# Optimization experiments

Hardware: AMD Instinct MI355X
Metric: run time of the kernel (lower is better)

The kernel has to match this reference:

```python
import jax, jax.numpy as jnp
import numpy as np

B, L, D, H, Dh = 4, 2048, 1024, 16, 64
DECAY_LR, A_LR, V_LR, G_LR = 64, 64, 32, 128
EPS_GN = 0.00064


def _lora(x, A, Bm, b, act):
    h = x @ A.T
    if act is not None:
        h = act(h)
    y = h @ Bm.T
    return y if b is None else y + b


def setup_inputs() -> dict:
    key = jax.random.key(0)
    ks = jax.random.split(key, 32)
    n = lambda k, shape, s=0.02: (jax.random.normal(k, shape, jnp.float32) * s)
    return {
        "x": n(ks[0], (B, L, D), 1.0),
        "v_first": n(ks[1], (B, L, H, Dh), 1.0),
        "x_r": n(ks[2], (1, 1, D)), "x_w": n(ks[3], (1, 1, D)),
        "x_k": n(ks[4], (1, 1, D)), "x_v": n(ks[5], (1, 1, D)),
        "x_a": n(ks[6], (1, 1, D)), "x_g": n(ks[7], (1, 1, D)),
        "k_k": n(ks[8], (H, Dh), 0.5), "k_a": n(ks[9], (H, Dh), 0.5),
        "r_k": n(ks[10], (H, Dh), 0.5),
        "Wr": n(ks[11], (D, D)), "Wk": n(ks[12], (D, D)),
        "Wv": n(ks[13], (D, D)), "Wo": n(ks[14], (D, D)),
        "gn_w": 1.0 + n(ks[15], (H, Dh)), "gn_b": n(ks[16], (H, Dh)),
        "w_A": n(ks[17], (DECAY_LR, D)), "w_B": n(ks[18], (D, DECAY_LR)), "w_b": n(ks[19], (D,)),
        "v_A": n(ks[20], (V_LR, D)), "v_B": n(ks[21], (D, V_LR)), "v_b": n(ks[22], (D,)),
        "a_A": n(ks[23], (A_LR, D)), "a_B": n(ks[24], (D, A_LR)), "a_b": n(ks[25], (D,)),
        "g_A": n(ks[26], (G_LR, D)), "g_B": n(ks[27], (D, G_LR)),
    }


def reference(x, v_first, x_r, x_w, x_k, x_v, x_a, x_g, k_k, k_a, r_k,
              Wr, Wk, Wv, Wo, gn_w, gn_b,
              w_A, w_B, w_b, v_A, v_B, v_b, a_A, a_B, a_b, g_A, g_B):
    Bx, Lx, Dx = x.shape
    # token shift (no cache -> zero-padded shift)
    x_prev = jnp.concatenate([jnp.zeros_like(x[:, :1]), x[:, :-1]], axis=1)
    xx = x_prev - x
    xr = x + xx * x_r
    xw = x + xx * x_w
    xk = x + xx * x_k
    xv = x + xx * x_v
    xa = x + xx * x_a
    xg = x + xx * x_g

    r = (xr @ Wr.T).reshape(Bx, Lx, H, Dh)
    k = (xk @ Wk.T).reshape(Bx, Lx, H, Dh)
    v = (xv @ Wv.T).reshape(Bx, Lx, H, Dh)
    iclr = jax.nn.sigmoid(_lora(xa, a_A, a_B, a_b, None)).reshape(Bx, Lx, H, Dh)
    gate = _lora(xg, g_A, g_B, None, jax.nn.sigmoid)  # (B,L,D)

    # layer_idx > 0: residual value mixing with v_first
    vv = jax.nn.sigmoid(_lora(xv, v_A, v_B, v_b, None)).reshape(Bx, Lx, H, Dh)
    v = v + (v_first - v) * vv

    w = jnp.exp(-0.606531 * jax.nn.sigmoid(
        _lora(xw, w_A, w_B, w_b, jnp.tanh)).reshape(Bx, Lx, H, Dh))

    kkn = k * k_k
    kk = kkn / jnp.maximum(jnp.linalg.norm(kkn, axis=-1, keepdims=True), 1e-7)
    k = k * (1.0 + (iclr - 1.0) * k_a)
    a = -kk
    b = kk * iclr

    # WKV7 generalized delta-rule scan over time
    def step(state, inp):
        rt, wt, kt, vt, at, bt = inp  # each (B,H,Dh)
        sa = jnp.einsum('bhij,bhj->bhi', state, at)
        state = (state * wt[:, :, None, :]
                 + vt[..., :, None] * kt[..., None, :]
                 + sa[..., :, None] * bt[..., None, :])
        y = jnp.einsum('bhij,bhj->bhi', state, rt)
        return state, y

    tr = lambda z: jnp.swapaxes(z, 0, 1)  # (B,L,H,Dh) -> (L,B,H,Dh)
    state0 = jnp.zeros((Bx, H, Dh, Dh), x.dtype)
    _, ys = jax.lax.scan(step, state0, (tr(r), tr(w), tr(k), tr(v), tr(a), tr(b)))
    out = jnp.swapaxes(ys, 0, 1)  # (B,L,H,Dh)

    # per-head layernorm (group norm), eps = 0.00064
    mean = out.mean(axis=-1, keepdims=True)
    var = out.var(axis=-1, keepdims=True)
    out = gn_w * (out - mean) / jnp.sqrt(var + EPS_GN) + gn_b

    out = out + jnp.sum(r * k * r_k, axis=-1, keepdims=True) * v
    out = out.reshape(Bx, Lx, Dx)
    return (out * gate) @ Wo.T
```

## Files before the change

### kernel.cpp

```cpp
#include <hip/hip_runtime.h>
#include <cmath>


#define DEV __device__ __forceinline__

typedef unsigned short u16;
typedef unsigned int u32;
typedef __bf16 bf16x8 __attribute__((ext_vector_type(8)));
typedef float f32x4 __attribute__((ext_vector_type(4)));

constexpr int Bx = 4, Lx = 2048, Dx = 1024, Hx = 16, Dh = 64;
constexpr int NTOK = Bx * Lx;
constexpr float EPS_GN = 0.00064f;
constexpr int STEP_U16 = 384;
constexpr int TB = 16;
constexpr int NB = Lx / TB;
constexpr int BATCH_U16 = TB * STEP_U16;

DEV float bf2f(u16 u) { union { u32 i; float f; } c; c.i = ((u32)u) << 16; return c.f; }
DEV u16 f2bf(float f) {
    union { float f; u32 i; } c; c.f = f;
    u32 r = c.i + 0x7FFFu + ((c.i >> 16) & 1u);
    return (u16)(r >> 16);
}
DEV void unpack2(u32 u, float& a, float& b) {
    union { u32 i; float f; } c0, c1;
    c0.i = u << 16; c1.i = u & 0xFFFF0000u;
    a = c0.f; b = c1.f;
}

template <int CTRL>
DEV float dpp_add(float v) {
    int p = __builtin_amdgcn_update_dpp(0, __float_as_int(v), CTRL, 0xF, 0xF, true);
    return v + __int_as_float(p);
}

DEV float xor32_add(float x) {
    float a = x, b = x;
    asm volatile("s_nop 1\n\tv_permlane32_swap_b32 %0, %1" : "+v"(a), "+v"(b));
    return a + b;
}

DEV float red32(float x) {
    x = dpp_add<0xB1>(x);
    x = dpp_add<0x4E>(x);
    x = dpp_add<0x141>(x);
    x = dpp_add<0x140>(x);
    return xor32_add(x);
}

__global__ __launch_bounds__(256) void conv_kernel(
    const float* s0, const float* s1, const float* s2, const float* s3,
    const float* s4, const float* s5, const float* s6, const float* s7,
    const float* s8, const float* s9, const float* s10, const float* s11,
    u16* d0, u16* d1, u16* d2, u16* d3, u16* d4, u16* d5, u16* d6, u16* d7,
    u16* d8, u16* d9, u16* d10, u16* d11)
{
    const float* srcs[12] = {s0,s1,s2,s3,s4,s5,s6,s7,s8,s9,s10,s11};
    u16* dsts[12] = {d0,d1,d2,d3,d4,d5,d6,d7,d8,d9,d10,d11};
    const int ns[12] = {65536,65536,32768,32768,65536,65536,131072,131072,
                        1048576,1048576,1048576,1048576};
    int t = blockIdx.y;
    int i = (blockIdx.x * 256 + threadIdx.x) * 4;
    if (i >= ns[t]) return;
    float4 v = *(const float4*)(srcs[t] + i);
    ushort4 o;
    o.x = f2bf(v.x); o.y = f2bf(v.y); o.z = f2bf(v.z); o.w = f2bf(v.w);
    *(ushort4*)(dsts[t] + i) = o;
}

__global__ __launch_bounds__(256) void mix_kernel(
    const float* __restrict__ x,
    const float* __restrict__ mr, const float* __restrict__ mw, const float* __restrict__ mk,
    const float* __restrict__ mv, const float* __restrict__ ma, const float* __restrict__ mg,
    u16* __restrict__ XR, u16* __restrict__ XW, u16* __restrict__ XK,
    u16* __restrict__ XV, u16* __restrict__ XA, u16* __restrict__ XG)
{
    int gi = blockIdx.x * 256 + threadIdx.x;
    int n  = gi >> 8;
    int d4 = (gi & 255) << 2;
    int l  = n & (Lx - 1);
    size_t o = (size_t)n * Dx + d4;
    float4 xc = *(const float4*)(x + o);
    float4 xp = make_float4(0.f, 0.f, 0.f, 0.f);
    if (l != 0) xp = *(const float4*)(x + o - Dx);
    float dx0 = xp.x - xc.x, dx1 = xp.y - xc.y, dx2 = xp.z - xc.z, dx3 = xp.w - xc.w;
    const float* mvs[6] = {mr, mw, mk, mv, ma, mg};
    u16* dsts[6] = {XR, XW, XK, XV, XA, XG};
#pragma unroll
    for (int j = 0; j < 6; ++j) {
        float4 m = *(const float4*)(mvs[j] + d4);
        ushort4 r;
        r.x = f2bf(fmaf(dx0, m.x, xc.x));
        r.y = f2bf(fmaf(dx1, m.y, xc.y));
        r.z = f2bf(fmaf(dx2, m.z, xc.z));
        r.w = f2bf(fmaf(dx3, m.w, xc.w));
        *(ushort4*)(dsts[j] + o) = r;
    }
}

template <int BN, int ACT, bool BIAS, bool F32OUT>
__global__ __launch_bounds__(256) void gemm_nt(
    const u16* __restrict__ A, const u16* __restrict__ B16,
    const float* __restrict__ bias, void* __restrict__ Cv,
    int M, int N, int K)
{
    constexpr int BM = 128, BK = 32;
    constexpr int LDT = BK + 8;
    constexpr int WGM = (BN == 128) ? 2 : 4;
    constexpr int WGN = (BN == 128) ? 2 : 1;
    constexpr int WTM = BM / WGM, WTN = BN / WGN;
    constexpr int ITM = WTM / 16, ITN = WTN / 16;
    __shared__ __align__(16) u16 Asm[BM * LDT];
    __shared__ __align__(16) u16 Bsm[BN * LDT];
    const int tid = threadIdx.x;
    const int wid = tid >> 6, lane = tid & 63;
    const int q = lane >> 4, r16 = lane & 15;
    const size_t m0 = (size_t)blockIdx.x * BM;
    const size_t n0 = (size_t)blockIdx.y * BN;
    const int wm = (wid % WGM) * WTM;
    const int wn = (wid / WGM) * WTN;
    f32x4 acc[ITM][ITN];
    const f32x4 zf = {0.f, 0.f, 0.f, 0.f};
#pragma unroll
    for (int i = 0; i < ITM; ++i)
#pragma unroll
        for (int j = 0; j < ITN; ++j) acc[i][j] = zf;

    for (int k0 = 0; k0 < K; k0 += BK) {
#pragma unroll
        for (int it = 0; it < (BM * BK) / 2048; ++it) {
            int pp = tid * 8 + it * 2048;
            int row = pp >> 5, col = pp & 31;
            *(uint4*)&Asm[row * LDT + col] = *(const uint4*)(A + (m0 + row) * K + k0 + col);
        }
#pragma unroll
        for (int it = 0; it < (BN * BK + 2047) / 2048; ++it) {
            int pp = tid * 8 + it * 2048;
            if (BN * BK >= 2048 || pp < BN * BK) {
                int row = pp >> 5, col = pp & 31;
                *(uint4*)&Bsm[row * LDT + col] = *(const uint4*)(B16 + (n0 + row) * K + k0 + col);
            }
        }
        __syncthreads();
        bf16x8 af[ITM], bfr[ITN];
#pragma unroll
        for (int im = 0; im < ITM; ++im)
            af[im] = *(const bf16x8*)&Asm[(wm + im * 16 + r16) * LDT + q * 8];
#pragma unroll
        for (int in = 0; in < ITN; ++in)
            bfr[in] = *(const bf16x8*)&Bsm[(wn + in * 16 + r16) * LDT + q * 8];
#pragma unroll
        for (int im = 0; im < ITM; ++im)
#pragma unroll
            for (int in = 0; in < ITN; ++in)
                acc[im][in] = __builtin_amdgcn_mfma_f32_16x16x32_bf16(af[im], bfr[in], acc[im][in], 0, 0, 0);
        __syncthreads();
    }
#pragma unroll
    for (int im = 0; im < ITM; ++im) {
#pragma unroll
        for (int in = 0; in < ITN; ++in) {
#pragma unroll
            for (int e = 0; e < 4; ++e) {
                size_t row = m0 + wm + im * 16 + q * 4 + e;
                size_t col = n0 + wn + in * 16 + r16;
                float val = acc[im][in][e];
                if constexpr (BIAS) val += bias[col];
                if constexpr (ACT == 1) val = 1.f / (1.f + __expf(-val));
                else if constexpr (ACT == 2) val = tanhf(val);
                else if constexpr (ACT == 3) val = __expf(-0.606531f / (1.f + __expf(-val)));
                if constexpr (F32OUT) ((float*)Cv)[row * (size_t)N + col] = val;
                else ((u16*)Cv)[row * (size_t)N + col] = f2bf(val);
            }
        }
    }
}

__global__ __launch_bounds__(256) void lora1_kernel(
    const u16* __restrict__ XW, const u16* __restrict__ XA,
    const u16* __restrict__ XV, const u16* __restrict__ XG,
    const u16* __restrict__ wAB, const u16* __restrict__ aAB,
    const u16* __restrict__ vAB, const u16* __restrict__ gAB,
    u16* __restrict__ HW, u16* __restrict__ HA,
    u16* __restrict__ HV, u16* __restrict__ HG)
{
    constexpr int BM = 128, BN = 64, BK = 32, K = 1024;
    constexpr int LDT = BK + 8;
    constexpr int ITM = 2, ITN = 4;
    const int cfg = blockIdx.y;
    const u16* A; const u16* Bm; u16* C; int ldC, Nv, act;
    if (cfg == 0)      { A = XW; Bm = wAB;            C = HW;      ldC = 64;  Nv = 64; act = 2; }
    else if (cfg == 1) { A = XA; Bm = aAB;            C = HA;      ldC = 64;  Nv = 64; act = 0; }
    else if (cfg == 2) { A = XV; Bm = vAB;            C = HV;      ldC = 32;  Nv = 32; act = 0; }
    else if (cfg == 3) { A = XG; Bm = gAB;            C = HG;      ldC = 128; Nv = 64; act = 1; }
    else               { A = XG; Bm = gAB + 64 * K;   C = HG + 64; ldC = 128; Nv = 64; act = 1; }

    __shared__ __align__(16) u16 Asm[BM * LDT];
    __shared__ __align__(16) u16 Bsm[BN * LDT];
    const int tid = threadIdx.x;
    const int wid = tid >> 6, lane = tid & 63;
    const int q = lane >> 4, r16 = lane & 15;
    const size_t m0 = (size_t)blockIdx.x * BM;
    const int wm = wid * 32;
    f32x4 acc[ITM][ITN];
    const f32x4 zf = {0.f, 0.f, 0.f, 0.f};
#pragma unroll
    for (int i = 0; i < ITM; ++i)
#pragma unroll
        for (int j = 0; j < ITN; ++j) acc[i][j] = zf;

    for (int k0 = 0; k0 < K; k0 += BK) {
#pragma unroll
        for (int it = 0; it < 2; ++it) {
            int pp = tid * 8 + it * 2048;
            int row = pp >> 5, col = pp & 31;
            *(uint4*)&Asm[row * LDT + col] = *(const uint4*)(A + (m0 + row) * K + k0 + col);
        }
        {
            int pp = tid * 8;
            int row = pp >> 5, col = pp & 31;
            *(uint4*)&Bsm[row * LDT + col] = *(const uint4*)(Bm + row * K + k0 + col);
        }
        __syncthreads();
        bf16x8 af[ITM], bfr[ITN];
#pragma unroll
        for (int im = 0; im < ITM; ++im)
            af[im] = *(const bf16x8*)&Asm[(wm + im * 16 + r16) * LDT + q * 8];
#pragma unroll
        for (int in = 0; in < ITN; ++in)
            bfr[in] = *(const bf16x8*)&Bsm[(in * 16 + r16) * LDT + q * 8];
#pragma unroll
        for (int im = 0; im < ITM; ++im)
#pragma unroll
            for (int in = 0; in < ITN; ++in)
                acc[im][in] = __builtin_amdgcn_mfma_f32_16x16x32_bf16(af[im], bfr[in], acc[im][in], 0, 0, 0);
        __syncthreads();
    }
#pragma unroll
    for (int im = 0; im < ITM; ++im) {
#pragma unroll
        for (int in = 0; in < ITN; ++in) {
#pragma unroll
            for (int e = 0; e < 4; ++e) {
                size_t row = m0 + wm + im * 16 + q * 4 + e;
                int col = in * 16 + r16;
                if (col < Nv) {
                    float val = acc[im][in][e];
                    if (act == 1) val = 1.f / (1.f + __expf(-val));
                    else if (act == 2) val = tanhf(val);
                    C[row * (size_t)ldC + col] = f2bf(val);
                }
            }
        }
    }
}

__global__ __launch_bounds__(256) void prep_pack_kernel(
    u16* __restrict__ Kb, u16* __restrict__ Vb,
    const u16* __restrict__ Rb, const u16* __restrict__ Wd16,
    const u16* __restrict__ ICLR, const u16* __restrict__ VVb, const float* __restrict__ vfirst,
    const float* __restrict__ k_k, const float* __restrict__ k_a,
    u16* __restrict__ stream)
{
    int g = blockIdx.x * 4 + (threadIdx.x >> 6);
    int lane = threadIdx.x & 63;
    int h = g & (Hx - 1);
    int n = g >> 4;
    size_t idx = (size_t)g * 64 + lane;
    int hd = h * 64 + lane;
    int l = n & (Lx - 1), b = n >> 11;
    size_t so = ((size_t)((b * 16 + h) * Lx + l)) * STEP_U16;

    float k = bf2f(Kb[idx]);
    float iclr = bf2f(ICLR[idx]);
    float kkn = k * k_k[hd];
    float s = kkn * kkn;
#pragma unroll
    for (int off = 32; off > 0; off >>= 1) s += __shfl_xor(s, off, 64);
    float nrm = fmaxf(sqrtf(s), 1e-7f);
    float kk = kkn / nrm;
    u16 knew = f2bf(k * (1.f + (iclr - 1.f) * k_a[hd]));
    float v = bf2f(Vb[idx]), vv = bf2f(VVb[idx]), vf = vfirst[idx];
    u16 vnew = f2bf(fmaf(vf - v, vv, v));
    Kb[idx] = knew;
    Vb[idx] = vnew;
    stream[so + lane]       = Rb[idx];
    stream[so + 64 + lane]  = knew;
    stream[so + 128 + lane] = f2bf(-kk);
    stream[so + 192 + lane] = f2bf(kk * iclr);
    stream[so + 256 + lane] = vnew;
    stream[so + 320 + lane] = Wd16[idx];
}

__global__ __launch_bounds__(256, 2) void scan_kernel(
    const u16* __restrict__ stream, float* __restrict__ Y)
{
    const int bid = blockIdx.x;
    const int xcd = bid & 7, slot = bid >> 3;
    const int bh = xcd + ((slot & 7) << 3);
    const int part = slot >> 3;
    const int tid = threadIdx.x;
    const int lane = tid & 63;
    const int w = tid >> 6;
    const int c = (lane & 15) | ((lane >> 1) & 16);
    const int rhalf = (lane >> 4) & 1;
    const int lr = w * 2 + rhalf;
    const int row = part * 8 + lr;
    const size_t sbase = (size_t)bh * Lx * STEP_U16;
    const size_t ybase = (size_t)(bh >> 4) * ((size_t)Lx * Dx) + (size_t)(bh & 15) * 64;

    __shared__ __align__(16) u16 sbuf[2 * BATCH_U16];
    __shared__ __align__(16) float yp[TB * 8 * 36];

    float S0 = 0.f, S1 = 0.f;

    {
        const u16* g = stream + sbase;
#pragma unroll
        for (int cc = 0; cc < 3; ++cc) {
            const u16* gp = g + (3 * w + cc) * 512 + lane * 8;
            u16* lp = sbuf + (3 * w + cc) * 512;
            __builtin_amdgcn_global_load_lds(
                (const __attribute__((address_space(1))) void*)gp,
                (__attribute__((address_space(3))) void*)lp, 16, 0, 0);
        }
    }

    for (int bt = 0; bt < NB; ++bt) {
        const int cur = bt & 1;
        __syncthreads();
        if (bt + 1 < NB) {
            const u16* g = stream + sbase + (size_t)(bt + 1) * BATCH_U16;
            u16* lbase = sbuf + (1 - cur) * BATCH_U16;
#pragma unroll
            for (int cc = 0; cc < 3; ++cc) {
                const u16* gp = g + (3 * w + cc) * 512 + lane * 8;
                u16* lp = lbase + (3 * w + cc) * 512;
                __builtin_amdgcn_global_load_lds(
                    (const __attribute__((address_space(1))) void*)gp,
                    (__attribute__((address_space(3))) void*)lp, 16, 0, 0);
            }
        }
        const u16* bp = sbuf + cur * BATCH_U16;
        const u16* cp = bp + c * 2;
        u32 r2 = *(const u32*)(cp);
        u32 k2 = *(const u32*)(cp + 64);
        u32 a2 = *(const u32*)(cp + 128);
        u32 b2 = *(const u32*)(cp + 192);
        u32 w2 = *(const u32*)(cp + 320);
        float v = bf2f(bp[256 + row]);
#pragma unroll
        for (int s = 0; s < TB; ++s) {
            u32 nr = 0, nk = 0, na = 0, nb = 0, nw = 0;
            float nv = 0.f;
            if (s + 1 < TB) {
                const u16* np = cp + (s + 1) * STEP_U16;
                nr = *(const u32*)(np);
                nk = *(const u32*)(np + 64);
                na = *(const u32*)(np + 128);
                nb = *(const u32*)(np + 192);
                nw = *(const u32*)(np + 320);
                nv = bf2f(bp[(s + 1) * STEP_U16 + 256 + row]);
            }
            float rr0, rr1, kk0, kk1, aa0, aa1, bb0, bb1, ww0, ww1;
            unpack2(r2, rr0, rr1);
            unpack2(k2, kk0, kk1);
            unpack2(a2, aa0, aa1);
            unpack2(b2, bb0, bb1);
            unpack2(w2, ww0, ww1);
            float sa = fmaf(S1, aa1, S0 * aa0);
            sa = red32(sa);
            float t0 = fmaf(v, kk0, sa * bb0);
            float t1 = fmaf(v, kk1, sa * bb1);
            S0 = fmaf(S0, ww0, t0);
            S1 = fmaf(S1, ww1, t1);
            float y = fmaf(S1, rr1, S0 * rr0);
            yp[(s * 8 + lr) * 36 + c] = y;
            r2 = nr; k2 = nk; a2 = na; b2 = nb; w2 = nw; v = nv;
        }
        __syncthreads();
        if (tid < TB * 8) {
            const float* rp = &yp[tid * 36];
            f32x4 a4 = *(const f32x4*)(rp);
#pragma unroll
            for (int i = 1; i < 8; ++i) {
                f32x4 t4 = *(const f32x4*)(rp + i * 4);
                a4 += t4;
            }
            float yy = (a4[0] + a4[1]) + (a4[2] + a4[3]);
            int s = tid >> 3, j = tid & 7;
            Y[ybase + (size_t)(bt * TB + s) * Dx + part * 8 + j] = yy;
        }
    }
}

__global__ __launch_bounds__(256) void gnorm_kernel(
    const float* __restrict__ Y, const u16* __restrict__ Rb, const u16* __restrict__ Kb,
    const u16* __restrict__ Vb, const float* __restrict__ r_k,
    const float* __restrict__ gnw, const float* __restrict__ gnb,
    u16* __restrict__ GATE_OG)
{
    int g = blockIdx.x * 4 + (threadIdx.x >> 6);
    int lane = threadIdx.x & 63;
    int h = g & (Hx - 1);
    size_t idx = (size_t)g * 64 + lane;
    int hd = h * 64 + lane;
    float y = Y[idx];
    float r = bf2f(Rb[idx]), k = bf2f(Kb[idx]), v = bf2f(Vb[idx]);
    float rkr = r * k * r_k[hd];
    float s1 = y, s2 = y * y, s3 = rkr;
#pragma unroll
    for (int off = 32; off > 0; off >>= 1) {
        s1 += __shfl_xor(s1, off, 64);
        s2 += __shfl_xor(s2, off, 64);
        s3 += __shfl_xor(s3, off, 64);
    }
    float mean = s1 * (1.f / 64.f);
    float var  = s2 * (1.f / 64.f) - mean * mean;
    float inv = 1.f / sqrtf(var + EPS_GN);
    float o = gnw[hd] * ((y - mean) * inv) + gnb[hd];
    o += s3 * v;
    GATE_OG[idx] = f2bf(o * bf2f(GATE_OG[idx]));
}

extern "C" void kernel_launch(void* const* d_in, const int* in_sizes, int n_in,
                              void* d_out, int out_size, void* d_ws, size_t ws_size,
                              hipStream_t stream_)
{
    const float* x      = (const float*)d_in[0];
    const float* vfirst = (const float*)d_in[1];
    const float* x_r = (const float*)d_in[2];
    const float* x_w = (const float*)d_in[3];
    const float* x_k = (const float*)d_in[4];
    const float* x_v = (const float*)d_in[5];
    const float* x_a = (const float*)d_in[6];
    const float* x_g = (const float*)d_in[7];
    const float* k_k = (const float*)d_in[8];
    const float* k_a = (const float*)d_in[9];
    const float* r_k = (const float*)d_in[10];
    const float* Wr  = (const float*)d_in[11];
    const float* Wk  = (const float*)d_in[12];
    const float* Wv  = (const float*)d_in[13];
    const float* Wo  = (const float*)d_in[14];
    const float* gnw = (const float*)d_in[15];
    const float* gnb = (const float*)d_in[16];
    const float* wA  = (const float*)d_in[17];
    const float* wB  = (const float*)d_in[18];
    const float* wb  = (const float*)d_in[19];
    const float* vA  = (const float*)d_in[20];
    const float* vB  = (const float*)d_in[21];
    const float* vb  = (const float*)d_in[22];
    const float* aA  = (const float*)d_in[23];
    const float* aB  = (const float*)d_in[24];
    const float* ab  = (const float*)d_in[25];
    const float* gA  = (const float*)d_in[26];
    const float* gB  = (const float*)d_in[27];

    char* ws = (char*)d_ws;
    const size_t SLOT = (size_t)NTOK * Dx * 2;
    u16* XR = (u16*)(ws + 0 * SLOT);
    u16* XW = (u16*)(ws + 1 * SLOT);
    u16* XK = (u16*)(ws + 2 * SLOT);
    u16* XV = (u16*)(ws + 3 * SLOT);
    u16* XA = (u16*)(ws + 4 * SLOT);
    u16* XG = (u16*)(ws + 5 * SLOT);
    u16* STREAM = (u16*)(ws + 0 * SLOT);
    u16* Rbuf = (u16*)(ws + 6 * SLOT);
    u16* Kbuf = (u16*)(ws + 7 * SLOT);
    u16* Vbuf = (u16*)(ws + 8 * SLOT);
    u16* HW = (u16*)(ws + 9 * SLOT);
    u16* HA = HW + (size_t)NTOK * 64;
    u16* HV = HA + (size_t)NTOK * 64;
    u16* HG = HV + (size_t)NTOK * 32;
    u16* Wo16 = HG + (size_t)NTOK * 128;
    u16* SW = (u16*)(ws + 9 * SLOT + 8 * 1024 * 1024);
    u16* wAB = SW;
    u16* wBB = wAB + 65536;
    u16* vAB = wBB + 65536;
    u16* vBB = vAB + 32768;
    u16* aAB = vBB + 32768;
    u16* aBB = aAB + 65536;
    u16* gAB = aBB + 65536;
    u16* gBB = gAB + 131072;
    u16* Wr16 = (u16*)(ws + 9 * SLOT + 10 * 1024 * 1024);
    u16* Wk16 = Wr16 + 1048576;
    u16* Wv16 = Wk16 + 1048576;
    u16* Wdec16 = (u16*)(ws + 10 * SLOT);
    u16* ICLR   = (u16*)(ws + 11 * SLOT);
    u16* VVb    = (u16*)(ws + 12 * SLOT);
    float* Yb   = (float*)(ws + 10 * SLOT);
    u16* GATE   = (u16*)(ws + 13 * SLOT);

    dim3 blk(256);
    conv_kernel<<<dim3(1024, 12), blk, 0, stream_>>>(
        wA, wB, vA, vB, aA, aB, gA, gB, Wr, Wk, Wv, Wo,
        wAB, wBB, vAB, vBB, aAB, aBB, gAB, gBB, Wr16, Wk16, Wv16, Wo16);
    mix_kernel<<<(NTOK * Dx / 4) / 256, blk, 0, stream_>>>(x, x_r, x_w, x_k, x_v, x_a, x_g,
                                                           XR, XW, XK, XV, XA, XG);
    gemm_nt<128, 0, false, false><<<dim3(64, 8), blk, 0, stream_>>>(XR, Wr16, nullptr, Rbuf, NTOK, 1024, 1024);
    gemm_nt<128, 0, false, false><<<dim3(64, 8), blk, 0, stream_>>>(XK, Wk16, nullptr, Kbuf, NTOK, 1024, 1024);
    gemm_nt<128, 0, false, false><<<dim3(64, 8), blk, 0, stream_>>>(XV, Wv16, nullptr, Vbuf, NTOK, 1024, 1024);
    lora1_kernel<<<dim3(64, 5), blk, 0, stream_>>>(XW, XA, XV, XG, wAB, aAB, vAB, gAB,
                                                   HW, HA, HV, HG);
    gemm_nt<128, 3, true,  false><<<dim3(64, 8), blk, 0, stream_>>>(HW, wBB, wb, Wdec16, NTOK, 1024, 64);
    gemm_nt<128, 1, true,  false><<<dim3(64, 8), blk, 0, stream_>>>(HA, aBB, ab, ICLR, NTOK, 1024, 64);
    gemm_nt<128, 1, true,  false><<<dim3(64, 8), blk, 0, stream_>>>(HV, vBB, vb, VVb, NTOK, 1024, 32);
    gemm_nt<128, 0, false, false><<<dim3(64, 8), blk, 0, stream_>>>(HG, gBB, nullptr, GATE, NTOK, 1024, 128);

    prep_pack_kernel<<<(NTOK * Hx) / 4, blk, 0, stream_>>>(Kbuf, Vbuf, Rbuf, Wdec16, ICLR, VVb,
                                                           vfirst, k_k, k_a, STREAM);
    scan_kernel<<<512, blk, 0, stream_>>>(STREAM, Yb);
    gnorm_kernel<<<(NTOK * Hx) / 4, blk, 0, stream_>>>(Yb, Rbuf, Kbuf, Vbuf, r_k, gnw, gnb, GATE);
    gemm_nt<128, 0, false, true><<<dim3(64, 8), blk, 0, stream_>>>(GATE, Wo16, nullptr, d_out, NTOK, 1024, 1024);
}
```

Before: 738.3 us.

## Load GEMM tiles directly into LDS and batch R/K/V projections in one launch

The GEMM and LoRA tile loads now use global_load_lds, which copies global memory straight into shared memory without going through registers. The padded LDS row stride is removed so the contiguous layout matches what that instruction writes. The three R/K/V projection GEMMs are merged into one launch indexed by blockIdx.z, which removes launch gaps and gives the GPU a larger grid to fill. Without the padding, the bf16x8 fragment reads may hit LDS bank conflicts, and there is still no double buffering.

```diff
diff --git a/kernel.cpp b/kernel.cpp
--- a/kernel.cpp
+++ b/kernel.cpp
@@ -100,24 +100,22 @@
 }
 
 template <int BN, int ACT, bool BIAS, bool F32OUT>
-__global__ __launch_bounds__(256) void gemm_nt(
-    const u16* __restrict__ A, const u16* __restrict__ B16,
-    const float* __restrict__ bias, void* __restrict__ Cv,
-    int M, int N, int K)
+DEV void gemm_body(const u16* __restrict__ A, const u16* __restrict__ B16,
+                   const float* __restrict__ bias, void* __restrict__ Cv,
+                   int M, int N, int K, int bx, int by)
 {
     constexpr int BM = 128, BK = 32;
-    constexpr int LDT = BK + 8;
     constexpr int WGM = (BN == 128) ? 2 : 4;
     constexpr int WGN = (BN == 128) ? 2 : 1;
     constexpr int WTM = BM / WGM, WTN = BN / WGN;
     constexpr int ITM = WTM / 16, ITN = WTN / 16;
-    __shared__ __align__(16) u16 Asm[BM * LDT];
-    __shared__ __align__(16) u16 Bsm[BN * LDT];
+    __shared__ __align__(16) u16 Asm[BM * BK];
+    __shared__ __align__(16) u16 Bsm[BN * BK];
     const int tid = threadIdx.x;
     const int wid = tid >> 6, lane = tid & 63;
     const int q = lane >> 4, r16 = lane & 15;
-    const size_t m0 = (size_t)blockIdx.x * BM;
-    const size_t n0 = (size_t)blockIdx.y * BN;
+    const size_t m0 = (size_t)bx * BM;
+    const size_t n0 = (size_t)by * BN;
     const int wm = (wid % WGM) * WTM;
     const int wn = (wid / WGM) * WTN;
     f32x4 acc[ITM][ITN];
@@ -129,27 +127,33 @@
 
     for (int k0 = 0; k0 < K; k0 += BK) {
 #pragma unroll
-        for (int it = 0; it < (BM * BK) / 2048; ++it) {
-            int pp = tid * 8 + it * 2048;
+        for (int it = 0; it < 2; ++it) {
+            int base = it * 2048 + wid * 512;
+            int pp = base + lane * 8;
             int row = pp >> 5, col = pp & 31;
-            *(uint4*)&Asm[row * LDT + col] = *(const uint4*)(A + (m0 + row) * K + k0 + col);
+            __builtin_amdgcn_global_load_lds(
+                (const __attribute__((address_space(1))) void*)(A + (m0 + row) * K + k0 + col),
+                (__attribute__((address_space(3))) void*)(Asm + base), 16, 0, 0);
         }
 #pragma unroll
         for (int it = 0; it < (BN * BK + 2047) / 2048; ++it) {
-            int pp = tid * 8 + it * 2048;
-            if (BN * BK >= 2048 || pp < BN * BK) {
+            int base = it * 2048 + wid * 512;
+            if (BN * BK >= 2048 || base < BN * BK) {
+                int pp = base + lane * 8;
                 int row = pp >> 5, col = pp & 31;
-                *(uint4*)&Bsm[row * LDT + col] = *(const uint4*)(B16 + (n0 + row) * K + k0 + col);
+                __builtin_amdgcn_global_load_lds(
+                    (const __attribute__((address_space(1))) void*)(B16 + (n0 + row) * K + k0 + col),
+                    (__attribute__((address_space(3))) void*)(Bsm + base), 16, 0, 0);
             }
         }
         __syncthreads();
         bf16x8 af[ITM], bfr[ITN];
 #pragma unroll
         for (int im = 0; im < ITM; ++im)
-            af[im] = *(const bf16x8*)&Asm[(wm + im * 16 + r16) * LDT + q * 8];
+            af[im] = *(const bf16x8*)&Asm[(wm + im * 16 + r16) * BK + q * 8];
 #pragma unroll
         for (int in = 0; in < ITN; ++in)
-            bfr[in] = *(const bf16x8*)&Bsm[(wn + in * 16 + r16) * LDT + q * 8];
+            bfr[in] = *(const bf16x8*)&Bsm[(wn + in * 16 + r16) * BK + q * 8];
 #pragma unroll
         for (int im = 0; im < ITM; ++im)
 #pragma unroll
@@ -177,6 +181,27 @@
     }
 }
 
+template <int BN, int ACT, bool BIAS, bool F32OUT>
+__global__ __launch_bounds__(256) void gemm_nt(
+    const u16* __restrict__ A, const u16* __restrict__ B16,
+    const float* __restrict__ bias, void* __restrict__ Cv,
+    int M, int N, int K)
+{
+    gemm_body<BN, ACT, BIAS, F32OUT>(A, B16, bias, Cv, M, N, K, blockIdx.x, blockIdx.y);
+}
+
+__global__ __launch_bounds__(256) void gemm_rkv_kernel(
+    const u16* __restrict__ XR, const u16* __restrict__ XK, const u16* __restrict__ XV,
+    const u16* __restrict__ Wr16, const u16* __restrict__ Wk16, const u16* __restrict__ Wv16,
+    u16* __restrict__ Rbuf, u16* __restrict__ Kbuf, u16* __restrict__ Vbuf)
+{
+    const u16* A; const u16* Bm; u16* C;
+    if (blockIdx.z == 0)      { A = XR; Bm = Wr16; C = Rbuf; }
+    else if (blockIdx.z == 1) { A = XK; Bm = Wk16; C = Kbuf; }
+    else                      { A = XV; Bm = Wv16; C = Vbuf; }
+    gemm_body<128, 0, false, false>(A, Bm, nullptr, C, NTOK, 1024, 1024, blockIdx.x, blockIdx.y);
+}
+
 __global__ __launch_bounds__(256) void lora1_kernel(
     const u16* __restrict__ XW, const u16* __restrict__ XA,
     const u16* __restrict__ XV, const u16* __restrict__ XG,
@@ -186,7 +211,6 @@
     u16* __restrict__ HV, u16* __restrict__ HG)
 {
     constexpr int BM = 128, BN = 64, BK = 32, K = 1024;
-    constexpr int LDT = BK + 8;
     constexpr int ITM = 2, ITN = 4;
     const int cfg = blockIdx.y;
     const u16* A; const u16* Bm; u16* C; int ldC, Nv, act;
@@ -196,8 +220,8 @@
     else if (cfg == 3) { A = XG; Bm = gAB;            C = HG;      ldC = 128; Nv = 64; act = 1; }
     else               { A = XG; Bm = gAB + 64 * K;   C = HG + 64; ldC = 128; Nv = 64; act = 1; }
 
-    __shared__ __align__(16) u16 Asm[BM * LDT];
-    __shared__ __align__(16) u16 Bsm[BN * LDT];
+    __shared__ __align__(16) u16 Asm[BM * BK];
+    __shared__ __align__(16) u16 Bsm[BN * BK];
     const int tid = threadIdx.x;
     const int wid = tid >> 6, lane = tid & 63;
     const int q = lane >> 4, r16 = lane & 15;
@@ -213,23 +237,29 @@
     for (int k0 = 0; k0 < K; k0 += BK) {
 #pragma unroll
         for (int it = 0; it < 2; ++it) {
-            int pp = tid * 8 + it * 2048;
+            int base = it * 2048 + wid * 512;
+            int pp = base + lane * 8;
             int row = pp >> 5, col = pp & 31;
-            *(uint4*)&Asm[row * LDT + col] = *(const uint4*)(A + (m0 + row) * K + k0 + col);
+            __builtin_amdgcn_global_load_lds(
+                (const __attribute__((address_space(1))) void*)(A + (m0 + row) * K + k0 + col),
+                (__attribute__((address_space(3))) void*)(Asm + base), 16, 0, 0);
         }
         {
-            int pp = tid * 8;
+            int base = wid * 512;
+            int pp = base + lane * 8;
             int row = pp >> 5, col = pp & 31;
-            *(uint4*)&Bsm[row * LDT + col] = *(const uint4*)(Bm + row * K + k0 + col);
+            __builtin_amdgcn_global_load_lds(
+                (const __attribute__((address_space(1))) void*)(Bm + row * K + k0 + col),
+                (__attribute__((address_space(3))) void*)(Bsm + base), 16, 0, 0);
         }
         __syncthreads();
         bf16x8 af[ITM], bfr[ITN];
 #pragma unroll
         for (int im = 0; im < ITM; ++im)
-            af[im] = *(const bf16x8*)&Asm[(wm + im * 16 + r16) * LDT + q * 8];
+            af[im] = *(const bf16x8*)&Asm[(wm + im * 16 + r16) * BK + q * 8];
 #pragma unroll
         for (int in = 0; in < ITN; ++in)
-            bfr[in] = *(const bf16x8*)&Bsm[(in * 16 + r16) * LDT + q * 8];
+            bfr[in] = *(const bf16x8*)&Bsm[(in * 16 + r16) * BK + q * 8];
 #pragma unroll
         for (int im = 0; im < ITM; ++im)
 #pragma unroll
@@ -498,9 +528,8 @@
         wAB, wBB, vAB, vBB, aAB, aBB, gAB, gBB, Wr16, Wk16, Wv16, Wo16);
     mix_kernel<<<(NTOK * Dx / 4) / 256, blk, 0, stream_>>>(x, x_r, x_w, x_k, x_v, x_a, x_g,
                                                            XR, XW, XK, XV, XA, XG);
-    gemm_nt<128, 0, false, false><<<dim3(64, 8), blk, 0, stream_>>>(XR, Wr16, nullptr, Rbuf, NTOK, 1024, 1024);
-    gemm_nt<128, 0, false, false><<<dim3(64, 8), blk, 0, stream_>>>(XK, Wk16, nullptr, Kbuf, NTOK, 1024, 1024);
-    gemm_nt<128, 0, false, false><<<dim3(64, 8), blk, 0, stream_>>>(XV, Wv16, nullptr, Vbuf, NTOK, 1024, 1024);
+    gemm_rkv_kernel<<<dim3(64, 8, 3), blk, 0, stream_>>>(XR, XK, XV, Wr16, Wk16, Wv16,
+                                                         Rbuf, Kbuf, Vbuf);
     lora1_kernel<<<dim3(64, 5), blk, 0, stream_>>>(XW, XA, XV, XG, wAB, aAB, vAB, gAB,
                                                    HW, HA, HV, HG);
     gemm_nt<128, 3, true,  false><<<dim3(64, 8), blk, 0, stream_>>>(HW, wBB, wb, Wdec16, NTOK, 1024, 64);
```

New measurement: 706.2 us. -4.3%, faster.
